# Kernel tuning notes

Measured on AMD Instinct MI355X. Metric: run time of the kernel, lower is better.

Reference implementation:

```python
import jax, jax.numpy as jnp
import numpy as np

NHEAD = 8
HEAD_DIM = 32  # per-head dim d; C = NHEAD * HEAD_DIM = 256
NEG_INF = -1e9


def setup_inputs() -> dict:
    key = jax.random.key(0)
    k1, k2, k3, k4, k5 = jax.random.split(key, 5)
    B, L, C = 8, 1024, NHEAD * HEAD_DIM
    query = jax.random.normal(k1, (B, L, C), dtype=jnp.float32)
    key_t = jax.random.normal(k2, (B, L, C), dtype=jnp.float32)
    value = jax.random.normal(k3, (B, L, C), dtype=jnp.float32)
    hard_mask = jax.random.randint(k4, (B, L), 0, 2).astype(bool)
    bias = jax.random.normal(k5, (B, L, L), dtype=jnp.float32)
    return {"query": query, "key": key_t, "value": value,
            "hard_mask": hard_mask, "bias": bias}


def reference(query, key, value, hard_mask, bias):
    # Faithful to the hard-mask path: attention is computed only among
    # active tokens (hard_mask True); inactive positions pass `value` through.
    # Masking inactive KEYS with -inf in the softmax is mathematically
    # identical to the sort/gather/slice/SDPA/scatter-unsort in the original.
    B, L, C = query.shape
    H, D = NHEAD, HEAD_DIM
    scale = 1.0 / jnp.sqrt(jnp.asarray(D, query.dtype))

    def split_heads(t):  # (B, L, C) -> (B, H, L, D)
        return t.reshape(B, L, H, D).transpose(0, 2, 1, 3)

    q, k, v = split_heads(query), split_heads(key), split_heads(value)

    # scores: (B, H, Lq, Lk); bias broadcasts over heads
    scores = jnp.einsum('bhld,bhmd->bhlm', q, k) * scale + bias[:, None, :, :]
    scores = jnp.where(hard_mask[:, None, None, :], scores, NEG_INF)
    attn = jax.nn.softmax(scores, axis=-1)
    out = jnp.einsum('bhlm,bhmd->bhld', attn, v)          # (B, H, L, D)
    out = out.transpose(0, 2, 1, 3).reshape(B, L, C)      # (B, L, C)

    # inactive query positions return the raw value (scatter-back behavior)
    out = jnp.where(hard_mask[:, :, None], out, value)

    # torch.stack over per-item (1, L, C) results -> (B, 1, L, C)
    return out[:, None, :, :]
```

## Files before the change

### kernel.cpp

```cpp
#include <hip/hip_runtime.h>

#define B_    8
#define H_    8
#define L_    1024
#define D_    32
#define C_    256
#define MQ    64
#define NK    64
#define KSTR  48
#define VSTR  72
#define PSTR  72

typedef __attribute__((ext_vector_type(8))) short bf16x8;
typedef __attribute__((ext_vector_type(4))) float f32x4;

__device__ inline unsigned short f2bf(float f) {
    union { float f; unsigned int u; } x; x.f = f;
    return (unsigned short)((x.u + 0x7fffu + ((x.u >> 16) & 1u)) >> 16);
}

__global__ __launch_bounds__(256) void masked_attn_mfma(
    const float* __restrict__ q,
    const float* __restrict__ k,
    const float* __restrict__ v,
    const int*   __restrict__ mask,
    const float* __restrict__ bias,
    float*       __restrict__ out)
{
    __shared__ __align__(16) unsigned short sQ[MQ][KSTR];
    __shared__ __align__(16) unsigned short sK[NK][KSTR];
    __shared__ __align__(16) unsigned short sVt[D_][VSTR];
    __shared__ __align__(16) unsigned short sP[4][16][PSTR];
    __shared__ float sMadd[NK];

    const int tid  = threadIdx.x;
    const int wv   = tid >> 6;
    const int ln   = tid & 63;
    const int l16  = ln & 15;
    const int quad = ln >> 4;

    const int blk = blockIdx.x;
    const int h   = blk & 7;
    const int qt  = (blk >> 3) & 15;
    const int b   = blk >> 7;
    const int q0  = qt * MQ;

    const float scale = 0.17677669529663687f;

    {
        const int row = tid >> 2, d0 = (tid & 3) * 8;
        const float* src = q + ((size_t)(b * L_ + q0 + row) * C_ + h * D_ + d0);
        float4 a = ((const float4*)src)[0];
        float4 c = ((const float4*)src)[1];
        __align__(16) unsigned short t8[8] = {
            f2bf(a.x), f2bf(a.y), f2bf(a.z), f2bf(a.w),
            f2bf(c.x), f2bf(c.y), f2bf(c.z), f2bf(c.w)};
        *(int4*)&sQ[row][d0] = *(const int4*)t8;
    }
    __syncthreads();

    const bf16x8 qfrag = *(const bf16x8*)&sQ[wv * 16 + l16][quad * 8];

    f32x4 Oacc[2] = {{0.f,0.f,0.f,0.f},{0.f,0.f,0.f,0.f}};
    float lsum[4] = {0.f, 0.f, 0.f, 0.f};

    for (int j0 = 0; j0 < L_; j0 += NK) {
        __syncthreads();
        {
            const int row = tid >> 2, d0 = (tid & 3) * 8;
            const size_t src = (size_t)(b * L_ + j0 + row) * C_ + h * D_ + d0;
            float4 ka = ((const float4*)(k + src))[0];
            float4 kb = ((const float4*)(k + src))[1];
            __align__(16) unsigned short t8[8] = {
                f2bf(ka.x), f2bf(ka.y), f2bf(ka.z), f2bf(ka.w),
                f2bf(kb.x), f2bf(kb.y), f2bf(kb.z), f2bf(kb.w)};
            *(int4*)&sK[row][d0] = *(const int4*)t8;

            float4 va = ((const float4*)(v + src))[0];
            float4 vb = ((const float4*)(v + src))[1];
            sVt[d0 + 0][row] = f2bf(va.x);
            sVt[d0 + 1][row] = f2bf(va.y);
            sVt[d0 + 2][row] = f2bf(va.z);
            sVt[d0 + 3][row] = f2bf(va.w);
            sVt[d0 + 4][row] = f2bf(vb.x);
            sVt[d0 + 5][row] = f2bf(vb.y);
            sVt[d0 + 6][row] = f2bf(vb.z);
            sVt[d0 + 7][row] = f2bf(vb.w);
            if (tid < NK) sMadd[tid] = mask[b * L_ + j0 + tid] ? 0.f : -1e9f;
        }
        __syncthreads();

        bf16x8 kf[4];
#pragma unroll
        for (int nt = 0; nt < 4; ++nt)
            kf[nt] = *(const bf16x8*)&sK[nt * 16 + l16][quad * 8];

        f32x4 S[4];
#pragma unroll
        for (int nt = 0; nt < 4; ++nt)
            S[nt] = __builtin_amdgcn_mfma_f32_16x16x32_bf16(
                qfrag, kf[nt], (f32x4){0.f,0.f,0.f,0.f}, 0, 0, 0);

        float psum[4] = {0.f, 0.f, 0.f, 0.f};
        const size_t brow0 = (size_t)(b * L_ + q0 + wv * 16 + quad * 4) * L_ + j0;
#pragma unroll
        for (int nt = 0; nt < 4; ++nt) {
            const float madd = sMadd[nt * 16 + l16];
#pragma unroll
            for (int r = 0; r < 4; ++r) {
                float s = S[nt][r] * scale + bias[brow0 + (size_t)r * L_ + nt * 16 + l16] + madd;
                float p = __expf(s);
                psum[r] += p;
                S[nt][r] = p;
            }
        }

#pragma unroll
        for (int nt = 0; nt < 4; ++nt)
#pragma unroll
            for (int r = 0; r < 4; ++r)
                sP[wv][quad * 4 + r][nt * 16 + l16] = f2bf(S[nt][r]);

#pragma unroll
        for (int r = 0; r < 4; ++r) {
            float t = psum[r];
            t += __shfl_xor(t, 1);
            t += __shfl_xor(t, 2);
            t += __shfl_xor(t, 4);
            t += __shfl_xor(t, 8);
            lsum[r] += t;
        }

#pragma unroll
        for (int s = 0; s < 2; ++s) {
            bf16x8 pf = *(const bf16x8*)&sP[wv][l16][s * 32 + quad * 8];
#pragma unroll
            for (int nt = 0; nt < 2; ++nt) {
                bf16x8 vf = *(const bf16x8*)&sVt[nt * 16 + l16][s * 32 + quad * 8];
                Oacc[nt] = __builtin_amdgcn_mfma_f32_16x16x32_bf16(pf, vf, Oacc[nt], 0, 0, 0);
            }
        }
    }

#pragma unroll
    for (int r = 0; r < 4; ++r) {
        const int qg = q0 + wv * 16 + quad * 4 + r;
        const int active = mask[b * L_ + qg];
        const size_t obase = (size_t)(b * L_ + qg) * C_ + h * D_;
        const float inv = 1.f / lsum[r];
#pragma unroll
        for (int nt = 0; nt < 2; ++nt) {
            float val;
            if (active) val = Oacc[nt][r] * inv;
            else        val = v[obase + nt * 16 + l16];
            out[obase + nt * 16 + l16] = val;
        }
    }
}

extern "C" void kernel_launch(void* const* d_in, const int* in_sizes, int n_in,
                              void* d_out, int out_size, void* d_ws, size_t ws_size,
                              hipStream_t stream) {
    const float* q    = (const float*)d_in[0];
    const float* k    = (const float*)d_in[1];
    const float* v    = (const float*)d_in[2];
    const int*   mask = (const int*)d_in[3];
    const float* bias = (const float*)d_in[4];
    float* out = (float*)d_out;

    dim3 grid(B_ * H_ * (L_ / MQ));
    dim3 block(256);
    masked_attn_mfma<<<grid, block, 0, stream>>>(q, k, v, mask, bias, out);
}
```

Baseline: 138.5 us.

## Precompute bf16 K and transposed V in workspace, stream them from global

A prep kernel converts K to bf16 and V to a transposed bf16 layout in the workspace once. The main attention kernel then reads these fragments straight from global/L2 instead of re-converting K/V per query tile through LDS with block-wide syncs. It uses smaller 128-thread blocks of 32 queries ordered head-major, and loads the full mask into LDS once. This removes redundant fp32 K/V loads and conversions plus the per-iteration barriers, at the cost of an extra launch and workspace traffic. The old kernel is kept as a fallback when the workspace is too small.

Result: slower. 163.3 us (+17.9%).

```diff
diff --git a/kernel.cpp b/kernel.cpp
--- a/kernel.cpp
+++ b/kernel.cpp
@@ -1,14 +1,12 @@
 #include <hip/hip_runtime.h>
+#include <hip/hip_bf16.h>
 
 #define B_    8
 #define H_    8
 #define L_    1024
 #define D_    32
 #define C_    256
-#define MQ    64
 #define NK    64
-#define KSTR  48
-#define VSTR  72
 #define PSTR  72
 
 typedef __attribute__((ext_vector_type(8))) short bf16x8;
@@ -18,6 +16,191 @@
     union { float f; unsigned int u; } x; x.f = f;
     return (unsigned short)((x.u + 0x7fffu + ((x.u >> 16) & 1u)) >> 16);
 }
+
+__device__ inline unsigned int pk_bf16(float lo, float hi) {
+    union { __hip_bfloat162 h; unsigned int u; } c;
+    c.h = __float22bfloat162_rn(make_float2(lo, hi));
+    return c.u;
+}
+
+__global__ __launch_bounds__(256) void prep_kv(
+    const float* __restrict__ k, const float* __restrict__ v,
+    unsigned short* __restrict__ kbf, unsigned short* __restrict__ vt)
+{
+    const int tid = threadIdx.x;
+    const int blk = blockIdx.x;
+    __shared__ float sTf[32][65];
+
+    if (blk < 1024) {
+        const size_t base = (size_t)blk * 2048 + (size_t)tid * 8;
+        float4 f0 = ((const float4*)(k + base))[0];
+        float4 f1 = ((const float4*)(k + base))[1];
+        uint4 o;
+        o.x = pk_bf16(f0.x, f0.y);
+        o.y = pk_bf16(f0.z, f0.w);
+        o.z = pk_bf16(f1.x, f1.y);
+        o.w = pk_bf16(f1.z, f1.w);
+        *(uint4*)(kbf + base) = o;
+    } else {
+        const int bid = blk - 1024;
+        const int bh = bid >> 4, g = bid & 15;
+        const int b = bh >> 3, h = bh & 7;
+        {
+            const int key = tid >> 2, d8 = (tid & 3) * 8;
+            const float* src = v + ((size_t)(b * L_ + g * 64 + key) * C_ + h * D_ + d8);
+            float4 a = ((const float4*)src)[0];
+            float4 c = ((const float4*)src)[1];
+            sTf[d8 + 0][key] = a.x; sTf[d8 + 1][key] = a.y;
+            sTf[d8 + 2][key] = a.z; sTf[d8 + 3][key] = a.w;
+            sTf[d8 + 4][key] = c.x; sTf[d8 + 5][key] = c.y;
+            sTf[d8 + 6][key] = c.z; sTf[d8 + 7][key] = c.w;
+        }
+        __syncthreads();
+        {
+            const int d = tid >> 3, seg = tid & 7;
+            uint4 o;
+            o.x = pk_bf16(sTf[d][seg * 8 + 0], sTf[d][seg * 8 + 1]);
+            o.y = pk_bf16(sTf[d][seg * 8 + 2], sTf[d][seg * 8 + 3]);
+            o.z = pk_bf16(sTf[d][seg * 8 + 4], sTf[d][seg * 8 + 5]);
+            o.w = pk_bf16(sTf[d][seg * 8 + 6], sTf[d][seg * 8 + 7]);
+            *(uint4*)(vt + ((size_t)(bh * D_ + d) * L_ + g * 64 + seg * 8)) = o;
+        }
+    }
+}
+
+__global__ __launch_bounds__(128, 4) void attn_main(
+    const float* __restrict__ q,
+    const float* __restrict__ v,
+    const int*   __restrict__ mask,
+    const float* __restrict__ bias,
+    const unsigned short* __restrict__ kbf,
+    const unsigned short* __restrict__ vt,
+    float*       __restrict__ out)
+{
+    __shared__ float sMadd[L_];
+    __shared__ __align__(16) unsigned short sP[2][16][PSTR];
+
+    const int tid  = threadIdx.x;
+    const int wv   = tid >> 6;
+    const int ln   = tid & 63;
+    const int l16  = ln & 15;
+    const int quad = ln >> 4;
+
+    const int blk = blockIdx.x;
+    const int h   = blk >> 8;
+    const int rem = blk & 255;
+    const int b   = rem >> 5;
+    const int qt  = rem & 31;
+    const int q0  = qt * 32 + wv * 16;
+
+    const float scale = 0.17677669529663687f;
+
+    {
+        const int4* mp = (const int4*)(mask + b * L_);
+        int4 m0 = mp[tid * 2], m1 = mp[tid * 2 + 1];
+        float* dst = &sMadd[tid * 8];
+        dst[0] = m0.x ? 0.f : -1e9f;
+        dst[1] = m0.y ? 0.f : -1e9f;
+        dst[2] = m0.z ? 0.f : -1e9f;
+        dst[3] = m0.w ? 0.f : -1e9f;
+        dst[4] = m1.x ? 0.f : -1e9f;
+        dst[5] = m1.y ? 0.f : -1e9f;
+        dst[6] = m1.z ? 0.f : -1e9f;
+        dst[7] = m1.w ? 0.f : -1e9f;
+    }
+    __syncthreads();
+
+    bf16x8 qfrag;
+    {
+        const float* qp = q + ((size_t)(b * L_ + q0 + l16) * C_ + h * D_ + quad * 8);
+        float4 a = ((const float4*)qp)[0];
+        float4 c = ((const float4*)qp)[1];
+        __align__(16) unsigned int u[4] = {
+            pk_bf16(a.x, a.y), pk_bf16(a.z, a.w),
+            pk_bf16(c.x, c.y), pk_bf16(c.z, c.w)};
+        qfrag = *(const bf16x8*)u;
+    }
+
+    f32x4 Oacc[2] = {{0.f,0.f,0.f,0.f},{0.f,0.f,0.f,0.f}};
+    float psum[4] = {0.f, 0.f, 0.f, 0.f};
+
+    const unsigned short* kbase = kbf + ((size_t)(b * L_) * C_ + h * D_ + quad * 8);
+    const unsigned short* vbase = vt + ((size_t)((b * H_ + h) * D_) * L_);
+    const size_t brow0 = (size_t)(b * L_ + q0 + quad * 4) * L_;
+
+    for (int j0 = 0; j0 < L_; j0 += NK) {
+        bf16x8 kf[4];
+#pragma unroll
+        for (int nt = 0; nt < 4; ++nt)
+            kf[nt] = *(const bf16x8*)(kbase + (size_t)(j0 + nt * 16 + l16) * C_);
+
+        f32x4 S[4];
+#pragma unroll
+        for (int nt = 0; nt < 4; ++nt)
+            S[nt] = __builtin_amdgcn_mfma_f32_16x16x32_bf16(
+                qfrag, kf[nt], (f32x4){0.f,0.f,0.f,0.f}, 0, 0, 0);
+
+        float madd[4];
+#pragma unroll
+        for (int nt = 0; nt < 4; ++nt)
+            madd[nt] = sMadd[j0 + nt * 16 + l16];
+
+#pragma unroll
+        for (int nt = 0; nt < 4; ++nt) {
+#pragma unroll
+            for (int r = 0; r < 4; ++r) {
+                float t = bias[brow0 + (size_t)r * L_ + j0 + nt * 16 + l16] + madd[nt];
+                float s = fmaf(S[nt][r], scale, t);
+                float p = __expf(s);
+                psum[r] += p;
+                S[nt][r] = p;
+            }
+        }
+
+#pragma unroll
+        for (int nt = 0; nt < 4; ++nt) {
+#pragma unroll
+            for (int r = 0; r < 4; r += 2) {
+                unsigned int u = pk_bf16(S[nt][r], S[nt][r + 1]);
+                sP[wv][quad * 4 + r    ][nt * 16 + l16] = (unsigned short)u;
+                sP[wv][quad * 4 + r + 1][nt * 16 + l16] = (unsigned short)(u >> 16);
+            }
+        }
+
+#pragma unroll
+        for (int s2 = 0; s2 < 2; ++s2) {
+            bf16x8 pf = *(const bf16x8*)&sP[wv][l16][s2 * 32 + quad * 8];
+#pragma unroll
+            for (int nt = 0; nt < 2; ++nt) {
+                bf16x8 vf = *(const bf16x8*)(vbase + (size_t)(nt * 16 + l16) * L_
+                                             + j0 + s2 * 32 + quad * 8);
+                Oacc[nt] = __builtin_amdgcn_mfma_f32_16x16x32_bf16(pf, vf, Oacc[nt], 0, 0, 0);
+            }
+        }
+    }
+
+#pragma unroll
+    for (int r = 0; r < 4; ++r) {
+        float t = psum[r];
+        t += __shfl_xor(t, 1);
+        t += __shfl_xor(t, 2);
+        t += __shfl_xor(t, 4);
+        t += __shfl_xor(t, 8);
+        const int qrow = q0 + quad * 4 + r;
+        const float inv = 1.f / t;
+        const bool active = (sMadd[qrow] == 0.f);
+        const size_t base = (size_t)(b * L_ + qrow) * C_ + h * D_;
+#pragma unroll
+        for (int nt = 0; nt < 2; ++nt) {
+            const size_t idx = base + nt * 16 + l16;
+            out[idx] = active ? Oacc[nt][r] * inv : v[idx];
+        }
+    }
+}
+
+#define MQ    64
+#define KSTR  48
+#define VSTR  72
 
 __global__ __launch_bounds__(256) void masked_attn_mfma(
     const float* __restrict__ q,
@@ -30,8 +213,8 @@
     __shared__ __align__(16) unsigned short sQ[MQ][KSTR];
     __shared__ __align__(16) unsigned short sK[NK][KSTR];
     __shared__ __align__(16) unsigned short sVt[D_][VSTR];
-    __shared__ __align__(16) unsigned short sP[4][16][PSTR];
-    __shared__ float sMadd[NK];
+    __shared__ __align__(16) unsigned short sP2[4][16][VSTR];
+    __shared__ float sMadd2[NK];
 
     const int tid  = threadIdx.x;
     const int wv   = tid >> 6;
@@ -86,7 +269,7 @@
             sVt[d0 + 5][row] = f2bf(vb.y);
             sVt[d0 + 6][row] = f2bf(vb.z);
             sVt[d0 + 7][row] = f2bf(vb.w);
-            if (tid < NK) sMadd[tid] = mask[b * L_ + j0 + tid] ? 0.f : -1e9f;
+            if (tid < NK) sMadd2[tid] = mask[b * L_ + j0 + tid] ? 0.f : -1e9f;
         }
         __syncthreads();
 
@@ -105,7 +288,7 @@
         const size_t brow0 = (size_t)(b * L_ + q0 + wv * 16 + quad * 4) * L_ + j0;
 #pragma unroll
         for (int nt = 0; nt < 4; ++nt) {
-            const float madd = sMadd[nt * 16 + l16];
+            const float madd = sMadd2[nt * 16 + l16];
 #pragma unroll
             for (int r = 0; r < 4; ++r) {
                 float s = S[nt][r] * scale + bias[brow0 + (size_t)r * L_ + nt * 16 + l16] + madd;
@@ -119,7 +302,7 @@
         for (int nt = 0; nt < 4; ++nt)
 #pragma unroll
             for (int r = 0; r < 4; ++r)
-                sP[wv][quad * 4 + r][nt * 16 + l16] = f2bf(S[nt][r]);
+                sP2[wv][quad * 4 + r][nt * 16 + l16] = f2bf(S[nt][r]);
 
 #pragma unroll
         for (int r = 0; r < 4; ++r) {
@@ -132,11 +315,11 @@
         }
 
 #pragma unroll
-        for (int s = 0; s < 2; ++s) {
-            bf16x8 pf = *(const bf16x8*)&sP[wv][l16][s * 32 + quad * 8];
+        for (int s2 = 0; s2 < 2; ++s2) {
+            bf16x8 pf = *(const bf16x8*)&sP2[wv][l16][s2 * 32 + quad * 8];
 #pragma unroll
             for (int nt = 0; nt < 2; ++nt) {
-                bf16x8 vf = *(const bf16x8*)&sVt[nt * 16 + l16][s * 32 + quad * 8];
+                bf16x8 vf = *(const bf16x8*)&sVt[nt * 16 + l16][s2 * 32 + quad * 8];
                 Oacc[nt] = __builtin_amdgcn_mfma_f32_16x16x32_bf16(pf, vf, Oacc[nt], 0, 0, 0);
             }
         }
@@ -168,7 +351,12 @@
     const float* bias = (const float*)d_in[4];
     float* out = (float*)d_out;
 
-    dim3 grid(B_ * H_ * (L_ / MQ));
-    dim3 block(256);
-    masked_attn_mfma<<<grid, block, 0, stream>>>(q, k, v, mask, bias, out);
-}
+    if (ws_size >= (size_t)8 * 1024 * 1024) {
+        unsigned short* kbf = (unsigned short*)d_ws;
+        unsigned short* vt  = kbf + (size_t)2 * 1024 * 1024;
+        prep_kv<<<2048, 256, 0, stream>>>(k, v, kbf, vt);
+        attn_main<<<2048, 128, 0, stream>>>(q, v, mask, bias, kbf, vt, out);
+    } else {
+        masked_attn_mfma<<<1024, 256, 0, stream>>>(q, k, v, mask, bias, out);
+    }
+}
```
